# Kernel optimization log

Measured on AMD Instinct MI355X. Metric: run time of the kernel, lower is better.

Reference implementation:

```python
import jax, jax.numpy as jnp
import numpy as np

N_NODES = 50000
N_EDGES = 800000
N_DEC = 1000000
D_IN, D_HID, D_OUT = 128, 128, 64


def setup_inputs() -> dict:
    key = jax.random.key(0)
    k = jax.random.split(key, 8)
    x = jax.random.normal(k[0], (N_NODES, D_IN), dtype=jnp.float32)
    # GCNConv linear weights (glorot-ish scale); bias added after aggregation (PyG default)
    W_in = jax.random.normal(k[1], (D_IN, D_HID), dtype=jnp.float32) / np.sqrt(D_IN)
    b_in = jnp.zeros((D_HID,), dtype=jnp.float32)
    W_out = jax.random.normal(k[2], (D_HID, D_OUT), dtype=jnp.float32) / np.sqrt(D_HID)
    b_out = jnp.zeros((D_OUT,), dtype=jnp.float32)
    edge_index = jax.random.randint(k[3], (2, N_EDGES), 0, N_NODES, dtype=jnp.int64)
    edge_label_index = jax.random.randint(k[4], (2, N_DEC), 0, N_NODES, dtype=jnp.int64)
    return {"x": x, "W_in": W_in, "b_in": b_in, "W_out": W_out, "b_out": b_out,
            "edge_index": edge_index, "edge_label_index": edge_label_index}


def reference(x, W_in, b_in, W_out, b_out, edge_index, edge_label_index):
    N = x.shape[0]
    # GCN normalization with self-loops (PyG GCNConv defaults)
    loop = jnp.arange(N, dtype=edge_index.dtype)
    src = jnp.concatenate([edge_index[0], loop])
    dst = jnp.concatenate([edge_index[1], loop])
    deg = jax.ops.segment_sum(jnp.ones_like(dst, dtype=x.dtype), dst, num_segments=N)
    dinv = jnp.where(deg > 0, jax.lax.rsqrt(jnp.maximum(deg, 1e-12)), 0.0)
    norm = (dinv[src] * dinv[dst])[:, None]  # [E+N, 1]

    def gcn(h, W, b):
        h = h @ W                                     # linear (no bias inside)
        agg = jax.ops.segment_sum(h[src] * norm, dst, num_segments=N)
        return agg + b                                # bias after aggregation

    z = jax.nn.relu(gcn(x, W_in, b_in))
    z = jax.nn.relu(gcn(z, W_out, b_out))
    # decoder: gather-multiply-sum over edge pairs -> logits [N_DEC]
    logits = jnp.sum(z[edge_label_index[0]] * z[edge_label_index[1]], axis=-1)
    return logits
```

## Files before the change

### kernel.cpp

```cpp
#include <hip/hip_runtime.h>

#define NN 50000
#define NE 800000
#define ND 1000000
#define DH 128
#define DO 64

#define NB 196
#define BCAP 5120
#define SCAP 6400
#define P1B 196
#define WTB1 25
#define GB1 ((NN + 63) / 64)

typedef _Float16 h16;
typedef h16 h16x4 __attribute__((ext_vector_type(4)));
typedef h16 h16x8 __attribute__((ext_vector_type(8)));
typedef float f32x4 __attribute__((ext_vector_type(4)));
typedef unsigned short u16;

__global__ __launch_bounds__(1024) void k_bucket_wt(
    const int* __restrict__ esrc, const int* __restrict__ edst,
    int* __restrict__ bpk, int* __restrict__ bcur,
    const float* __restrict__ Wi, const float* __restrict__ Wo,
    h16* __restrict__ WiT, h16* __restrict__ WoT,
    h16* __restrict__ h1, h16* __restrict__ h2) {
    if (blockIdx.x < P1B) {
        __shared__ int hist[NB], gbase[NB], lcur[NB];
        int t = threadIdx.x;
        if (t < NB) { hist[t] = 0; lcur[t] = 0; }
        __syncthreads();
        int base = blockIdx.x * 4096;
        int b[4], pk[4];
#pragma unroll
        for (int i = 0; i < 4; ++i) {
            int idx = base + t + i * 1024;
            if (idx < NE) {
                int s = esrc[idx];
                int d = edst[idx];
                b[i] = d >> 8;
                pk[i] = s | ((d & 255) << 16);
                atomicAdd(&hist[b[i]], 1);
            } else {
                b[i] = -1;
            }
        }
        __syncthreads();
        if (t < NB && hist[t] > 0) gbase[t] = atomicAdd(&bcur[t], hist[t]);
        __syncthreads();
#pragma unroll
        for (int i = 0; i < 4; ++i) {
            if (b[i] >= 0) {
                int r = atomicAdd(&lcur[b[i]], 1);
                bpk[b[i] * BCAP + gbase[b[i]] + r] = pk[i];
            }
        }
    } else {
        int t = (blockIdx.x - P1B) * 1024 + threadIdx.x;
        if (t < 128 * 128) {
            int k = t >> 7, n = t & 127;
            WiT[n * 128 + k] = (h16)Wi[t];
        } else if (t < 128 * 128 + 64 * 128) {
            int t2 = t - 128 * 128;
            int k = t2 >> 6, n = t2 & 63;
            WoT[n * 128 + k] = (h16)Wo[t2];
        } else if (t < 128 * 128 + 64 * 128 + 192) {
            int t3 = t - (128 * 128 + 64 * 128);
            if (t3 < 128) h1[(size_t)NN * DH + t3] = (h16)0.f;
            else          h2[(size_t)NN * DO + (t3 - 128)] = (h16)0.f;
        }
    }
}

template <int BN, bool AF32>
__device__ __forceinline__ void gemm_body(
    const void* __restrict__ Ain, const h16* __restrict__ WT,
    h16* __restrict__ out, int bx, char* sX, char* sW) {
    const int tid = threadIdx.x;
    const int row0 = bx * 64;

#pragma unroll
    for (int i = 0; i < 4; ++i) {
        int c = tid + i * 256;
        int row = c >> 4, kb = c & 15;
        int gr = row0 + row;
        h16x8 v = {};
        if (gr < NN) {
            if (AF32) {
                const float* src = (const float*)Ain + (size_t)gr * 128 + kb * 8;
                float4 u0 = *(const float4*)src;
                float4 u1 = *(const float4*)(src + 4);
                v[0] = (h16)u0.x; v[1] = (h16)u0.y; v[2] = (h16)u0.z; v[3] = (h16)u0.w;
                v[4] = (h16)u1.x; v[5] = (h16)u1.y; v[6] = (h16)u1.z; v[7] = (h16)u1.w;
            } else {
                v = *(const h16x8*)((const h16*)Ain + (size_t)gr * 128 + kb * 8);
            }
        }
        *(h16x8*)(sX + row * 256 + ((kb * 16) ^ ((row & 7) << 4))) = v;
    }
#pragma unroll
    for (int i = 0; i < BN / 16; ++i) {
        int c = tid + i * 256;
        int n = c >> 4, kb = c & 15;
        h16x8 v = *(const h16x8*)&WT[(size_t)n * 128 + kb * 8];
        *(h16x8*)(sW + n * 256 + ((kb * 16) ^ ((n & 7) << 4))) = v;
    }
    __syncthreads();

    const int lane = tid & 63, wv = tid >> 6;
    const int g = lane >> 4, l15 = lane & 15;
    const int r = wv * 16 + l15;
    f32x4 acc[BN / 16];
#pragma unroll
    for (int ct = 0; ct < BN / 16; ++ct) acc[ct] = (f32x4){0.f, 0.f, 0.f, 0.f};

#pragma unroll
    for (int t = 0; t < 4; ++t) {
        int kb2 = t * 64 + g * 16;
        h16x8 a = *(const h16x8*)(sX + r * 256 + (kb2 ^ ((r & 7) << 4)));
#pragma unroll
        for (int ct = 0; ct < BN / 16; ++ct) {
            int n = ct * 16 + l15;
            h16x8 b = *(const h16x8*)(sW + n * 256 + (kb2 ^ ((n & 7) << 4)));
            acc[ct] = __builtin_amdgcn_mfma_f32_16x16x32_f16(a, b, acc[ct], 0, 0, 0);
        }
    }

#pragma unroll
    for (int j = 0; j < 4; ++j) {
        int row = row0 + wv * 16 + g * 4 + j;
        if (row < NN) {
#pragma unroll
            for (int ct = 0; ct < BN / 16; ++ct)
                out[(size_t)row * BN + ct * 16 + l15] = (h16)acc[ct][j];
        }
    }
}

__global__ __launch_bounds__(256) void k_sort_gemm1(
    const int* __restrict__ bpk, const int* __restrict__ bcur,
    int* __restrict__ gcur, int* __restrict__ off, int* __restrict__ degn,
    float* __restrict__ dinv, u16* __restrict__ csrc,
    const float* __restrict__ x, const h16* __restrict__ WiT,
    h16* __restrict__ h1) {
    __shared__ __align__(16) char smem[49152];
    if (blockIdx.x >= NB) {
        gemm_body<DH, true>(x, WiT, h1, blockIdx.x - NB, smem, smem + 16384);
        return;
    }
    int* hist = (int*)smem;
    int* lofs = hist + 256;
    int* exc  = lofs + 256;
    int* lcur = exc + 256;
    int* sgb  = lcur + 256;
    u16* scsr = (u16*)(sgb + 4);
    int b = blockIdx.x, t = threadIdx.x;
    hist[t] = 0; lcur[t] = 0;
    __syncthreads();
    int cnt = bcur[b];
    const int* bp = bpk + b * BCAP;
    for (int j = t; j < cnt; j += 256)
        atomicAdd(&hist[(bp[j] >> 16) & 255], 1);
    __syncthreads();
    int pd = (hist[t] + 7) & ~7;
    lofs[t] = pd;
    __syncthreads();
#pragma unroll
    for (int d = 1; d < 256; d <<= 1) {
        int add = (t >= d) ? lofs[t - d] : 0;
        __syncthreads();
        lofs[t] += add;
        __syncthreads();
    }
    exc[t] = lofs[t] - pd;
    __syncthreads();
    int cntp = lofs[255];
    if (t == 0) *sgb = atomicAdd(gcur, cntp);
    for (int j = t; j < cntp; j += 256) scsr[j] = (u16)NN;
    __syncthreads();
    int gbase = *sgb;
    int node = b * 256 + t;
    if (node < NN) {
        off[node] = gbase + exc[t];
        degn[node] = pd;
        dinv[node] = rsqrtf((float)hist[t] + 1.0f);
    }
    if (b == 0 && t == 0) dinv[NN] = 0.f;
    for (int j = t; j < cnt; j += 256) {
        int p = bp[j];
        int d = (p >> 16) & 255;
        int r = atomicAdd(&lcur[d], 1);
        scsr[exc[d] + r] = (u16)(p & 0xFFFF);
    }
    __syncthreads();
    u16* cdst = csrc + gbase;
    for (int j = t; j < cntp / 2; j += 256)
        *(unsigned*)(cdst + 2 * j) = *(const unsigned*)(scsr + 2 * j);
}

__global__ __launch_bounds__(256) void k_gemm2(
    const h16* __restrict__ z1, const h16* __restrict__ WoT,
    h16* __restrict__ h2) {
    __shared__ __align__(16) char smem[32768];
    gemm_body<DO, false>(z1, WoT, h2, blockIdx.x, smem, smem + 16384);
}

__global__ __launch_bounds__(256) void k_agg128(
    const h16x4* __restrict__ hs, const float* __restrict__ dinv,
    const int* __restrict__ off, const int* __restrict__ degn,
    const u16* __restrict__ csrc,
    const float* __restrict__ bias, h16x4* __restrict__ z) {
    int node = blockIdx.x * 8 + (threadIdx.x >> 5);
    if (node >= NN) return;
    int col = threadIdx.x & 31;
    int s = off[node], e = s + degn[node];
    float a0 = 0.f, a1 = 0.f, a2 = 0.f, a3 = 0.f;
    for (int j = s; j < e; j += 8) {
        int i0 = csrc[j],     i1 = csrc[j + 1], i2 = csrc[j + 2], i3 = csrc[j + 3];
        int i4 = csrc[j + 4], i5 = csrc[j + 5], i6 = csrc[j + 6], i7 = csrc[j + 7];
        float w0 = dinv[i0], w1 = dinv[i1], w2 = dinv[i2], w3 = dinv[i3];
        float w4 = dinv[i4], w5 = dinv[i5], w6 = dinv[i6], w7 = dinv[i7];
        h16x4 v0 = hs[(size_t)i0 * 32 + col];
        h16x4 v1 = hs[(size_t)i1 * 32 + col];
        h16x4 v2 = hs[(size_t)i2 * 32 + col];
        h16x4 v3 = hs[(size_t)i3 * 32 + col];
        h16x4 v4 = hs[(size_t)i4 * 32 + col];
        h16x4 v5 = hs[(size_t)i5 * 32 + col];
        h16x4 v6 = hs[(size_t)i6 * 32 + col];
        h16x4 v7 = hs[(size_t)i7 * 32 + col];
        a0 = fmaf(w0, (float)v0.x, a0); a1 = fmaf(w0, (float)v0.y, a1);
        a2 = fmaf(w0, (float)v0.z, a2); a3 = fmaf(w0, (float)v0.w, a3);
        a0 = fmaf(w1, (float)v1.x, a0); a1 = fmaf(w1, (float)v1.y, a1);
        a2 = fmaf(w1, (float)v1.z, a2); a3 = fmaf(w1, (float)v1.w, a3);
        a0 = fmaf(w2, (float)v2.x, a0); a1 = fmaf(w2, (float)v2.y, a1);
        a2 = fmaf(w2, (float)v2.z, a2); a3 = fmaf(w2, (float)v2.w, a3);
        a0 = fmaf(w3, (float)v3.x, a0); a1 = fmaf(w3, (float)v3.y, a1);
        a2 = fmaf(w3, (float)v3.z, a2); a3 = fmaf(w3, (float)v3.w, a3);
        a0 = fmaf(w4, (float)v4.x, a0); a1 = fmaf(w4, (float)v4.y, a1);
        a2 = fmaf(w4, (float)v4.z, a2); a3 = fmaf(w4, (float)v4.w, a3);
        a0 = fmaf(w5, (float)v5.x, a0); a1 = fmaf(w5, (float)v5.y, a1);
        a2 = fmaf(w5, (float)v5.z, a2); a3 = fmaf(w5, (float)v5.w, a3);
        a0 = fmaf(w6, (float)v6.x, a0); a1 = fmaf(w6, (float)v6.y, a1);
        a2 = fmaf(w6, (float)v6.z, a2); a3 = fmaf(w6, (float)v6.w, a3);
        a0 = fmaf(w7, (float)v7.x, a0); a1 = fmaf(w7, (float)v7.y, a1);
        a2 = fmaf(w7, (float)v7.z, a2); a3 = fmaf(w7, (float)v7.w, a3);
    }
    float dv = dinv[node];
    h16x4 vs = hs[(size_t)node * 32 + col];
    a0 = fmaf(dv, (float)vs.x, a0); a1 = fmaf(dv, (float)vs.y, a1);
    a2 = fmaf(dv, (float)vs.z, a2); a3 = fmaf(dv, (float)vs.w, a3);
    float4 bb = ((const float4*)bias)[col];
    float r0 = dv * a0 + bb.x, r1 = dv * a1 + bb.y;
    float r2 = dv * a2 + bb.z, r3 = dv * a3 + bb.w;
    h16x4 o;
    o.x = (h16)(r0 > 0.f ? r0 : 0.f); o.y = (h16)(r1 > 0.f ? r1 : 0.f);
    o.z = (h16)(r2 > 0.f ? r2 : 0.f); o.w = (h16)(r3 > 0.f ? r3 : 0.f);
    z[(size_t)node * 32 + col] = o;
}

__global__ __launch_bounds__(256) void k_agg64(
    const h16x4* __restrict__ hs, const float* __restrict__ dinv,
    const int* __restrict__ off, const int* __restrict__ degn,
    const u16* __restrict__ csrc,
    const float* __restrict__ bias, h16x4* __restrict__ z) {
    int node = blockIdx.x * 16 + (threadIdx.x >> 4);
    if (node >= NN) return;
    int col = threadIdx.x & 15;
    int s = off[node], e = s + degn[node];
    float a0 = 0.f, a1 = 0.f, a2 = 0.f, a3 = 0.f;
    for (int j = s; j < e; j += 8) {
        int i0 = csrc[j],     i1 = csrc[j + 1], i2 = csrc[j + 2], i3 = csrc[j + 3];
        int i4 = csrc[j + 4], i5 = csrc[j + 5], i6 = csrc[j + 6], i7 = csrc[j + 7];
        float w0 = dinv[i0], w1 = dinv[i1], w2 = dinv[i2], w3 = dinv[i3];
        float w4 = dinv[i4], w5 = dinv[i5], w6 = dinv[i6], w7 = dinv[i7];
        h16x4 v0 = hs[(size_t)i0 * 16 + col];
        h16x4 v1 = hs[(size_t)i1 * 16 + col];
        h16x4 v2 = hs[(size_t)i2 * 16 + col];
        h16x4 v3 = hs[(size_t)i3 * 16 + col];
        h16x4 v4 = hs[(size_t)i4 * 16 + col];
        h16x4 v5 = hs[(size_t)i5 * 16 + col];
        h16x4 v6 = hs[(size_t)i6 * 16 + col];
        h16x4 v7 = hs[(size_t)i7 * 16 + col];
        a0 = fmaf(w0, (float)v0.x, a0); a1 = fmaf(w0, (float)v0.y, a1);
        a2 = fmaf(w0, (float)v0.z, a2); a3 = fmaf(w0, (float)v0.w, a3);
        a0 = fmaf(w1, (float)v1.x, a0); a1 = fmaf(w1, (float)v1.y, a1);
        a2 = fmaf(w1, (float)v1.z, a2); a3 = fmaf(w1, (float)v1.w, a3);
        a0 = fmaf(w2, (float)v2.x, a0); a1 = fmaf(w2, (float)v2.y, a1);
        a2 = fmaf(w2, (float)v2.z, a2); a3 = fmaf(w2, (float)v2.w, a3);
        a0 = fmaf(w3, (float)v3.x, a0); a1 = fmaf(w3, (float)v3.y, a1);
        a2 = fmaf(w3, (float)v3.z, a2); a3 = fmaf(w3, (float)v3.w, a3);
        a0 = fmaf(w4, (float)v4.x, a0); a1 = fmaf(w4, (float)v4.y, a1);
        a2 = fmaf(w4, (float)v4.z, a2); a3 = fmaf(w4, (float)v4.w, a3);
        a0 = fmaf(w5, (float)v5.x, a0); a1 = fmaf(w5, (float)v5.y, a1);
        a2 = fmaf(w5, (float)v5.z, a2); a3 = fmaf(w5, (float)v5.w, a3);
        a0 = fmaf(w6, (float)v6.x, a0); a1 = fmaf(w6, (float)v6.y, a1);
        a2 = fmaf(w6, (float)v6.z, a2); a3 = fmaf(w6, (float)v6.w, a3);
        a0 = fmaf(w7, (float)v7.x, a0); a1 = fmaf(w7, (float)v7.y, a1);
        a2 = fmaf(w7, (float)v7.z, a2); a3 = fmaf(w7, (float)v7.w, a3);
    }
    float dv = dinv[node];
    h16x4 vs = hs[(size_t)node * 16 + col];
    a0 = fmaf(dv, (float)vs.x, a0); a1 = fmaf(dv, (float)vs.y, a1);
    a2 = fmaf(dv, (float)vs.z, a2); a3 = fmaf(dv, (float)vs.w, a3);
    float4 bb = ((const float4*)bias)[col];
    float r0 = dv * a0 + bb.x, r1 = dv * a1 + bb.y;
    float r2 = dv * a2 + bb.z, r3 = dv * a3 + bb.w;
    h16x4 o;
    o.x = (h16)(r0 > 0.f ? r0 : 0.f); o.y = (h16)(r1 > 0.f ? r1 : 0.f);
    o.z = (h16)(r2 > 0.f ? r2 : 0.f); o.w = (h16)(r3 > 0.f ? r3 : 0.f);
    z[(size_t)node * 16 + col] = o;
}

__global__ __launch_bounds__(256) void k_dec(const h16* __restrict__ z2,
                                             const int* __restrict__ eli,
                                             float* __restrict__ out) {
    int g = blockIdx.x * 32 + (threadIdx.x >> 3);
    int p0 = g * 8;
    if (p0 >= ND) return;
    int sub = threadIdx.x & 7;
    int4 ea0 = *(const int4*)&eli[p0];
    int4 ea1 = *(const int4*)&eli[p0 + 4];
    int4 eb0 = *(const int4*)&eli[ND + p0];
    int4 eb1 = *(const int4*)&eli[ND + p0 + 4];
    int ia[8] = {ea0.x, ea0.y, ea0.z, ea0.w, ea1.x, ea1.y, ea1.z, ea1.w};
    int ib[8] = {eb0.x, eb0.y, eb0.z, eb0.w, eb1.x, eb1.y, eb1.z, eb1.w};
    float v[8];
#pragma unroll
    for (int q = 0; q < 8; ++q) {
        h16x8 va = *(const h16x8*)&z2[(size_t)ia[q] * DO + sub * 8];
        h16x8 vb = *(const h16x8*)&z2[(size_t)ib[q] * DO + sub * 8];
        float acc = 0.f;
#pragma unroll
        for (int k = 0; k < 8; ++k) acc += (float)va[k] * (float)vb[k];
        v[q] = acc;
    }
#pragma unroll
    for (int o = 1; o < 8; o <<= 1) {
#pragma unroll
        for (int q = 0; q < 8; ++q) v[q] += __shfl_xor(v[q], o);
    }
    if (sub == 0) {
        *(float4*)&out[p0] = make_float4(v[0], v[1], v[2], v[3]);
        *(float4*)&out[p0 + 4] = make_float4(v[4], v[5], v[6], v[7]);
    }
}

extern "C" void kernel_launch(void* const* d_in, const int* in_sizes, int n_in,
                              void* d_out, int out_size, void* d_ws, size_t ws_size,
                              hipStream_t stream) {
    const float* x  = (const float*)d_in[0];
    const float* Wi = (const float*)d_in[1];
    const float* bi = (const float*)d_in[2];
    const float* Wo = (const float*)d_in[3];
    const float* bo = (const float*)d_in[4];
    const int* ei   = (const int*)d_in[5];
    const int* eli  = (const int*)d_in[6];
    float* out = (float*)d_out;

    char* ws = (char*)d_ws;
    size_t o = 0;
    auto alloc = [&](size_t bytes) -> char* {
        char* p = ws + o;
        o = (o + bytes + 255) & ~(size_t)255;
        return p;
    };
    float* dinv = (float*)alloc((NN + 1) * 4);
    int* bcur   = (int*)alloc((NB + 1) * 4);
    int* off    = (int*)alloc(NN * 4);
    int* degn   = (int*)alloc(NN * 4);
    int* bpk    = (int*)alloc((size_t)NB * BCAP * 4);
    u16* csrc   = (u16*)alloc(((size_t)NE + 8 * NN + 64) * 2);
    h16* WiT    = (h16*)alloc(128 * 128 * 2);
    h16* WoT    = (h16*)alloc(64 * 128 * 2);
    h16* h1     = (h16*)alloc((size_t)(NN + 1) * DH * 2);
    h16* z1     = (h16*)alloc((size_t)NN * DH * 2);
    h16* h2     = (h16*)alloc((size_t)(NN + 1) * DO * 2);
    h16* z2     = (h16*)alloc((size_t)NN * DO * 2);

    const int* esrc = ei;
    const int* edst = ei + NE;

    hipMemsetAsync(bcur, 0, (NB + 1) * 4, stream);
    k_bucket_wt<<<P1B + WTB1, 1024, 0, stream>>>(esrc, edst, bpk, bcur, Wi, Wo,
                                                 WiT, WoT, h1, h2);
    k_sort_gemm1<<<NB + GB1, 256, 0, stream>>>(bpk, bcur, &bcur[NB], off, degn,
                                               dinv, csrc, x, WiT, h1);
    k_agg128<<<(NN + 7) / 8, 256, 0, stream>>>((const h16x4*)h1, dinv, off, degn, csrc, bi, (h16x4*)z1);
    k_gemm2<<<GB1, 256, 0, stream>>>(z1, WoT, h2);
    k_agg64<<<(NN + 15) / 16, 256, 0, stream>>>((const h16x4*)h2, dinv, off, degn, csrc, bo, (h16x4*)z2);

    k_dec<<<(ND / 8 + 31) / 32, 256, 0, stream>>>(z2, eli, out);
}
```

Measured before the change: 110.6 us.

## Replace global atomic bucketing with per-block slots and fixed CSR offsets

```diff
diff --git a/kernel.cpp b/kernel.cpp
--- a/kernel.cpp
+++ b/kernel.cpp
@@ -7,8 +7,7 @@
 #define DO 64
 
 #define NB 196
-#define BCAP 5120
-#define SCAP 6400
+#define BCAPP 6400
 #define P1B 196
 #define WTB1 25
 #define GB1 ((NN + 63) / 64)
@@ -21,40 +20,30 @@
 
 __global__ __launch_bounds__(1024) void k_bucket_wt(
     const int* __restrict__ esrc, const int* __restrict__ edst,
-    int* __restrict__ bpk, int* __restrict__ bcur,
+    int* __restrict__ bpk, int* __restrict__ cnt,
     const float* __restrict__ Wi, const float* __restrict__ Wo,
     h16* __restrict__ WiT, h16* __restrict__ WoT,
     h16* __restrict__ h1, h16* __restrict__ h2) {
     if (blockIdx.x < P1B) {
-        __shared__ int hist[NB], gbase[NB], lcur[NB];
+        __shared__ int lcur[NB];
         int t = threadIdx.x;
-        if (t < NB) { hist[t] = 0; lcur[t] = 0; }
+        if (t < NB) lcur[t] = 0;
         __syncthreads();
         int base = blockIdx.x * 4096;
-        int b[4], pk[4];
 #pragma unroll
         for (int i = 0; i < 4; ++i) {
             int idx = base + t + i * 1024;
             if (idx < NE) {
                 int s = esrc[idx];
                 int d = edst[idx];
-                b[i] = d >> 8;
-                pk[i] = s | ((d & 255) << 16);
-                atomicAdd(&hist[b[i]], 1);
-            } else {
-                b[i] = -1;
+                int bb = d >> 8;
+                int r = atomicAdd(&lcur[bb], 1);
+                bpk[((size_t)bb * P1B + blockIdx.x) * 64 + r] =
+                    s | ((d & 255) << 16);
             }
         }
         __syncthreads();
-        if (t < NB && hist[t] > 0) gbase[t] = atomicAdd(&bcur[t], hist[t]);
-        __syncthreads();
-#pragma unroll
-        for (int i = 0; i < 4; ++i) {
-            if (b[i] >= 0) {
-                int r = atomicAdd(&lcur[b[i]], 1);
-                bpk[b[i] * BCAP + gbase[b[i]] + r] = pk[i];
-            }
-        }
+        if (t < NB) cnt[blockIdx.x * NB + t] = lcur[t];
     } else {
         int t = (blockIdx.x - P1B) * 1024 + threadIdx.x;
         if (t < 128 * 128) {
@@ -138,8 +127,8 @@
 }
 
 __global__ __launch_bounds__(256) void k_sort_gemm1(
-    const int* __restrict__ bpk, const int* __restrict__ bcur,
-    int* __restrict__ gcur, int* __restrict__ off, int* __restrict__ degn,
+    const int* __restrict__ bpk, const int* __restrict__ cnt,
+    int* __restrict__ off, int* __restrict__ degn,
     float* __restrict__ dinv, u16* __restrict__ csrc,
     const float* __restrict__ x, const h16* __restrict__ WiT,
     h16* __restrict__ h1) {
@@ -148,19 +137,34 @@
         gemm_body<DH, true>(x, WiT, h1, blockIdx.x - NB, smem, smem + 16384);
         return;
     }
-    int* hist = (int*)smem;
-    int* lofs = hist + 256;
-    int* exc  = lofs + 256;
-    int* lcur = exc + 256;
-    int* sgb  = lcur + 256;
-    u16* scsr = (u16*)(sgb + 4);
+    int* hist   = (int*)smem;
+    int* lofs   = hist + 256;
+    int* exc    = lofs + 256;
+    int* lcur   = exc + 256;
+    int* cbs    = lcur + 256;
+    int* scsr32 = cbs + 256;
+    u16* scsr16 = (u16*)(scsr32 + 5120);
     int b = blockIdx.x, t = threadIdx.x;
     hist[t] = 0; lcur[t] = 0;
-    __syncthreads();
-    int cnt = bcur[b];
-    const int* bp = bpk + b * BCAP;
-    for (int j = t; j < cnt; j += 256)
-        atomicAdd(&hist[(bp[j] >> 16) & 255], 1);
+    int cc = (t < P1B) ? cnt[t * NB + b] : 0;
+    cbs[t] = cc;
+    __syncthreads();
+#pragma unroll
+    for (int d = 1; d < 256; d <<= 1) {
+        int add = (t >= d) ? cbs[t - d] : 0;
+        __syncthreads();
+        cbs[t] += add;
+        __syncthreads();
+    }
+    int cbase = cbs[t] - cc;
+    int craw = cbs[255];
+    if (t < P1B) {
+        const int* src = bpk + ((size_t)b * P1B + t) * 64;
+        for (int i = 0; i < cc; ++i) scsr32[cbase + i] = src[i];
+    }
+    __syncthreads();
+    for (int j = t; j < craw; j += 256)
+        atomicAdd(&hist[(scsr32[j] >> 16) & 255], 1);
     __syncthreads();
     int pd = (hist[t] + 7) & ~7;
     lofs[t] = pd;
@@ -175,27 +179,25 @@
     exc[t] = lofs[t] - pd;
     __syncthreads();
     int cntp = lofs[255];
-    if (t == 0) *sgb = atomicAdd(gcur, cntp);
-    for (int j = t; j < cntp; j += 256) scsr[j] = (u16)NN;
-    __syncthreads();
-    int gbase = *sgb;
+    for (int j = t; j < cntp; j += 256) scsr16[j] = (u16)NN;
+    __syncthreads();
     int node = b * 256 + t;
     if (node < NN) {
-        off[node] = gbase + exc[t];
+        off[node] = b * BCAPP + exc[t];
         degn[node] = pd;
         dinv[node] = rsqrtf((float)hist[t] + 1.0f);
     }
     if (b == 0 && t == 0) dinv[NN] = 0.f;
-    for (int j = t; j < cnt; j += 256) {
-        int p = bp[j];
+    for (int j = t; j < craw; j += 256) {
+        int p = scsr32[j];
         int d = (p >> 16) & 255;
         int r = atomicAdd(&lcur[d], 1);
-        scsr[exc[d] + r] = (u16)(p & 0xFFFF);
-    }
-    __syncthreads();
-    u16* cdst = csrc + gbase;
+        scsr16[exc[d] + r] = (u16)(p & 0xFFFF);
+    }
+    __syncthreads();
+    u16* cdst = csrc + (size_t)b * BCAPP;
     for (int j = t; j < cntp / 2; j += 256)
-        *(unsigned*)(cdst + 2 * j) = *(const unsigned*)(scsr + 2 * j);
+        *(unsigned*)(cdst + 2 * j) = *(const unsigned*)(scsr16 + 2 * j);
 }
 
 __global__ __launch_bounds__(256) void k_gemm2(
@@ -365,11 +367,11 @@
         return p;
     };
     float* dinv = (float*)alloc((NN + 1) * 4);
-    int* bcur   = (int*)alloc((NB + 1) * 4);
     int* off    = (int*)alloc(NN * 4);
     int* degn   = (int*)alloc(NN * 4);
-    int* bpk    = (int*)alloc((size_t)NB * BCAP * 4);
-    u16* csrc   = (u16*)alloc(((size_t)NE + 8 * NN + 64) * 2);
+    int* cnt    = (int*)alloc((size_t)P1B * NB * 4);
+    int* bpk    = (int*)alloc((size_t)NB * P1B * 64 * 4);
+    u16* csrc   = (u16*)alloc((size_t)NB * BCAPP * 2);
     h16* WiT    = (h16*)alloc(128 * 128 * 2);
     h16* WoT    = (h16*)alloc(64 * 128 * 2);
     h16* h1     = (h16*)alloc((size_t)(NN + 1) * DH * 2);
@@ -380,10 +382,9 @@
     const int* esrc = ei;
     const int* edst = ei + NE;
 
-    hipMemsetAsync(bcur, 0, (NB + 1) * 4, stream);
-    k_bucket_wt<<<P1B + WTB1, 1024, 0, stream>>>(esrc, edst, bpk, bcur, Wi, Wo,
+    k_bucket_wt<<<P1B + WTB1, 1024, 0, stream>>>(esrc, edst, bpk, cnt, Wi, Wo,
                                                  WiT, WoT, h1, h2);
-    k_sort_gemm1<<<NB + GB1, 256, 0, stream>>>(bpk, bcur, &bcur[NB], off, degn,
+    k_sort_gemm1<<<NB + GB1, 256, 0, stream>>>(bpk, cnt, off, degn,
                                                dinv, csrc, x, WiT, h1);
     k_agg128<<<(NN + 7) / 8, 256, 0, stream>>>((const h16x4*)h1, dinv, off, degn, csrc, bi, (h16x4*)z1);
     k_gemm2<<<GB1, 256, 0, stream>>>(z1, WoT, h2);
```

Result: faster. 95.99 us, median of 2 (-13.2%).
